# Kernel tuning notes

Hardware: AMD Instinct MI355X
Metric: run time of the kernel (lower is better)

The kernel has to match this reference:

```python
import jax, jax.numpy as jnp
import numpy as np

N = 10000   # num nodes
E = 160000  # num edges (avg degree 16)
B = 8       # batch dim carried on node state
D = 64      # hidden_size


def setup_inputs() -> dict:
    key = jax.random.key(0)
    k1, k2, k3, k4, k5, k6 = jax.random.split(key, 6)
    state = jax.random.normal(k1, (N, B, D), jnp.float32)
    feature = jax.random.normal(k2, (N, 32), jnp.float32)  # unused by GAT math, kept for call signature
    weight = jax.random.normal(k3, (2 * D, D), jnp.float32) * 0.05
    src = jax.random.randint(k4, (E,), 0, N, jnp.int32)
    dst = jax.random.randint(k5, (E,), 0, N, jnp.int32)
    dist = jax.random.uniform(k6, (E, 1), jnp.float32)
    return dict(state=state, feature=feature, weight=weight, src=src, dst=dst, dist=dist)


def reference(state, feature, weight, src, dst, dist):
    # --- msg_edge: gather src/dst node states per edge ---
    src_state = state[src]                 # [E,B,D]
    dst_state = state[dst]                 # [E,B,D]
    es = jnp.concatenate([src_state, dst_state], axis=-1)          # [E,B,2D]
    alpha = jax.nn.leaky_relu(jnp.einsum('ebk,kd->ebd', es, weight),
                              negative_slope=0.2)                  # tf.nn.leaky_relu alpha=0.2
    alpha = alpha * dist[:, :, None]       # dist [E,1] broadcast to [E,1,1]

    # --- msg_reduce: segment softmax over incoming edges of each dst node ---
    amax = jax.ops.segment_max(alpha, dst, num_segments=N)         # [N,B,D]
    ex = jnp.exp(alpha - amax[dst])                                # stable exp
    denom = jax.ops.segment_sum(ex, dst, num_segments=N)           # [N,B,D]
    attn = ex / denom[dst]                                         # [E,B,D]

    # weighted sum of src states scattered back to dst nodes, then relu
    new_state = jax.nn.relu(jax.ops.segment_sum(attn * src_state, dst, num_segments=N))
    return new_state
```

## Files before the change

### kernel.cpp

```cpp
#include <hip/hip_runtime.h>
#include <hip/hip_fp16.h>
#include <math.h>

#define N_NODES 10000
#define N_EDGES 160000
#define B_ 8
#define D_ 64
#define BD 512
#define ROWS 80000
#define SLICE 640000
#define CAP 48

typedef _Float16 f16x8 __attribute__((ext_vector_type(8)));
typedef float f32x4 __attribute__((ext_vector_type(4)));
typedef float f4v __attribute__((ext_vector_type(4)));
typedef unsigned int u32;

union HU { _Float16 f; unsigned short u; };
union HC { u32 u; __half2 h; };

__global__ void __launch_bounds__(256) prep_kernel(
    const int* __restrict__ src, const int* __restrict__ dst,
    const float* __restrict__ dist, int* __restrict__ counts, u32* __restrict__ bucket,
    const float* __restrict__ state, const float* __restrict__ weight,
    __half2* __restrict__ G, __half* __restrict__ Pd) {
    __shared__ _Float16 At[64 * 72];
    __shared__ _Float16 Bt[128 * 72];
    int bid = blockIdx.x;
    int tid = threadIdx.x;

    if (bid < 625) {
        int e = bid * 256 + tid;
        int s = __builtin_nontemporal_load(&src[e]);
        int d = __builtin_nontemporal_load(&dst[e]);
        float di = __builtin_nontemporal_load(&dist[e]);
        int pos = atomicAdd(&counts[d], 1);
        if (pos < CAP) {
            unsigned short hd = __half_as_ushort(__float2half_rn(di * 1.44269504f));
            bucket[d * CAP + pos] = (u32)s | ((u32)hd << 16);
        }
        return;
    }

    int row0 = (bid - 625) * 64;

    const f4v* st4 = (const f4v*)(state + (size_t)row0 * 64);
    for (int i = tid; i < 1024; i += 256) {
        int r = i >> 4, c4 = (i & 15) << 2;
        f4v v = __builtin_nontemporal_load(&st4[i]);
        union { short4 s; _Float16 h[4]; } u;
        u.h[0] = (_Float16)v[0]; u.h[1] = (_Float16)v[1];
        u.h[2] = (_Float16)v[2]; u.h[3] = (_Float16)v[3];
        *(short4*)&At[r * 72 + c4] = u.s;
    }
    const f4v* w4 = (const f4v*)weight;
    for (int i = tid; i < 2048; i += 256) {
        int r = i >> 4, c4 = (i & 15) << 2;
        f4v v = w4[i];
        int h = r >> 6, k = r & 63;
        int nb = h * 64 + c4;
        Bt[(nb + 0) * 72 + k] = (_Float16)v[0];
        Bt[(nb + 1) * 72 + k] = (_Float16)v[1];
        Bt[(nb + 2) * 72 + k] = (_Float16)v[2];
        Bt[(nb + 3) * 72 + k] = (_Float16)v[3];
    }
    __syncthreads();

    int wave = tid >> 6, lane = tid & 63;
    int quad = lane >> 4, m16 = lane & 15;
    int m_loc = wave * 16 + m16;

    f16x8 a0 = *(const f16x8*)&At[m_loc * 72 + quad * 8];
    f16x8 a1 = *(const f16x8*)&At[m_loc * 72 + 32 + quad * 8];

#pragma unroll
    for (int tcol = 0; tcol < 8; tcol++) {
        int n = tcol * 16 + m16;
        f16x8 b0 = *(const f16x8*)&Bt[n * 72 + quad * 8];
        f16x8 b1 = *(const f16x8*)&Bt[n * 72 + 32 + quad * 8];
        f32x4 acc = {0.f, 0.f, 0.f, 0.f};
        acc = __builtin_amdgcn_mfma_f32_16x16x32_f16(a0, b0, acc, 0, 0, 0);
        acc = __builtin_amdgcn_mfma_f32_16x16x32_f16(a1, b1, acc, 0, 0, 0);
#pragma unroll
        for (int r = 0; r < 4; r++) {
            int ml = wave * 16 + quad * 4 + r;
            int m = row0 + ml;
            int node = m >> 3, bb = m & 7;
            size_t base = (size_t)bb * SLICE + (size_t)node * 64;
            if (tcol < 4) {
                HU xu; xu.f = At[ml * 72 + n];
                ushort2 pk;
                pk.x = __half_as_ushort(__float2half_rn(acc[r]));
                pk.y = xu.u;
                *(ushort2*)&G[base + n] = pk;
            } else {
                Pd[base + (n - 64)] = __float2half_rn(acc[r]);
            }
        }
    }
}

__global__ void __launch_bounds__(256) gat_aggregate(
    const __half2* __restrict__ G,
    const __half* __restrict__ Pds,
    const int* __restrict__ counts,
    const u32* __restrict__ bucket,
    float* __restrict__ out) {
    int bid = blockIdx.x;
    int b = bid & 7;
    int grp = bid >> 3;
    int wave = threadIdx.x >> 6;
    int lane = threadIdx.x & 63;
    int n = (grp << 2) + wave;
    int eidx = lane >> 4;
    int lpart = lane & 15;

    const __half2* Gb = G + (size_t)b * SLICE;
    const __half* Pb = Pds + (size_t)b * SLICE;

    union { double d; __half2 h[2]; } pdu;
    pdu.d = __builtin_nontemporal_load((const double*)(Pb + n * 64 + lpart * 4));
    __half2 pd01 = pdu.h[0], pd23 = pdu.h[1];

    int cnt = counts[n];
    if (cnt > CAP) cnt = CAP;
    const u32* ep = bucket + n * CAP;

    const __half2 c06 = __float2half2_rn(0.6f);
    const __half2 c04 = __float2half2_rn(0.4f);
    const u32 ABSM = 0x7fff7fffu;

    __half2 l01 = __float2half2_rn(0.f), l23 = l01;
    __half2 o01 = l01, o23 = l01;

    if (cnt > 0) {
        int last = cnt - 1;
        int idx = eidx <= last ? eidx : last;
        u32 rec = __builtin_nontemporal_load(&ep[idx]);
        float4 g = *(const float4*)(Gb + (size_t)(rec & 0xffffu) * 64 + lpart * 4);
        __half hdd = __ushort_as_half((unsigned short)(rec >> 16));
        __half2 ddl = __halves2half2(hdd, hdd);
        int j = 0;
        for (;;) {
            int jn = j + 4;
            bool more = jn < cnt;
            float4 g2; __half2 ddl2;
            if (more) {
                int i2 = jn + eidx; i2 = i2 <= last ? i2 : last;
                u32 rec2 = __builtin_nontemporal_load(&ep[i2]);
                g2 = *(const float4*)(Gb + (size_t)(rec2 & 0xffffu) * 64 + lpart * 4);
                __half h2 = __ushort_as_half((unsigned short)(rec2 >> 16));
                ddl2 = __halves2half2(h2, h2);
            }
            bool act = (j + eidx) <= last;
            union { float4 f; __half2 h[4]; } gu; gu.f = g;
            __half2 p01 = __halves2half2(__low2half(gu.h[0]), __low2half(gu.h[1]));
            __half2 p23 = __halves2half2(__low2half(gu.h[2]), __low2half(gu.h[3]));
            __half2 x01 = __halves2half2(__high2half(gu.h[0]), __high2half(gu.h[1]));
            __half2 x23 = __halves2half2(__high2half(gu.h[2]), __high2half(gu.h[3]));
            __half2 z01 = __hadd2(p01, pd01);
            __half2 z23 = __hadd2(p23, pd23);
            HC az01, az23, zz01, zz23;
            zz01.h = z01; zz23.h = z23;
            az01.u = zz01.u & ABSM;
            az23.u = zz23.u & ABSM;
            __half2 lk01 = __hfma2(az01.h, c04, __hmul2(z01, c06));
            __half2 lk23 = __hfma2(az23.h, c04, __hmul2(z23, c06));
            __half2 a01 = __hmul2(lk01, ddl);
            __half2 a23 = __hmul2(lk23, ddl);
            __half2 e01 = __halves2half2(hexp2(__low2half(a01)), hexp2(__high2half(a01)));
            __half2 e23 = __halves2half2(hexp2(__low2half(a23)), hexp2(__high2half(a23)));
            HC s01, s23;
            s01.h = e01; s23.h = e23;
            s01.u = act ? s01.u : 0u;
            s23.u = act ? s23.u : 0u;
            l01 = __hadd2(l01, s01.h);
            l23 = __hadd2(l23, s23.h);
            o01 = __hfma2(s01.h, x01, o01);
            o23 = __hfma2(s23.h, x23, o23);
            if (!more) break;
            j = jn; g = g2; ddl = ddl2;
        }
#pragma unroll
        for (int m = 16; m <= 32; m <<= 1) {
            HC c;
            c.u = (u32)__shfl_xor((int)((HC){.h = l01}).u, m, 64); l01 = __hadd2(l01, c.h);
            c.u = (u32)__shfl_xor((int)((HC){.h = l23}).u, m, 64); l23 = __hadd2(l23, c.h);
            c.u = (u32)__shfl_xor((int)((HC){.h = o01}).u, m, 64); o01 = __hadd2(o01, c.h);
            c.u = (u32)__shfl_xor((int)((HC){.h = o23}).u, m, 64); o23 = __hadd2(o23, c.h);
        }
    }
    if (eidx == 0) {
        f4v r;
        if (cnt > 0) {
            float l0 = __low2float(l01), l1 = __high2float(l01);
            float l2 = __low2float(l23), l3 = __high2float(l23);
            float o0 = __low2float(o01), o1 = __high2float(o01);
            float o2 = __low2float(o23), o3 = __high2float(o23);
            r[0] = fmaxf(o0 * __builtin_amdgcn_rcpf(l0), 0.f);
            r[1] = fmaxf(o1 * __builtin_amdgcn_rcpf(l1), 0.f);
            r[2] = fmaxf(o2 * __builtin_amdgcn_rcpf(l2), 0.f);
            r[3] = fmaxf(o3 * __builtin_amdgcn_rcpf(l3), 0.f);
        } else {
            r[0] = 0.f; r[1] = 0.f; r[2] = 0.f; r[3] = 0.f;
        }
        f4v* dst4 = (f4v*)(out + (size_t)n * BD + b * 64 + lpart * 4);
        __builtin_nontemporal_store(r, dst4);
    }
}

extern "C" void kernel_launch(void* const* d_in, const int* in_sizes, int n_in,
                              void* d_out, int out_size, void* d_ws, size_t ws_size,
                              hipStream_t stream) {
    const float* state  = (const float*)d_in[0];
    const float* weight = (const float*)d_in[2];
    const int*   src    = (const int*)d_in[3];
    const int*   dst    = (const int*)d_in[4];
    const float* dist   = (const float*)d_in[5];

    __half2* G      = (__half2*)d_ws;
    __half*  Pd     = (__half*)(G + (size_t)8 * SLICE);
    u32*     bucket = (u32*)(Pd + (size_t)8 * SLICE);
    int*     counts = (int*)(bucket + (size_t)N_NODES * CAP);

    hipMemsetAsync(counts, 0, N_NODES * sizeof(int), stream);
    prep_kernel<<<1875, 256, 0, stream>>>(src, dst, dist, counts, bucket,
                                          state, weight, G, Pd);
    gat_aggregate<<<N_NODES * 2, 256, 0, stream>>>(G, Pd, counts, bucket, (float*)d_out);
}
```

Baseline: 164.3 us.

## Stage GEMM outputs in LDS for vector stores, unroll gather by eight edges

The prep kernel now writes MFMA results into shared-memory tiles and then emits coalesced 16-byte stores to G and Pd, replacing scattered 4-byte and 2-byte stores. The aggregate kernel handles eight edges per iteration with two in-flight gathers per lane, raising memory-level parallelism at the cost of more registers. Nontemporal load and store hints are dropped in favour of ordinary loads and stores. The extra shared memory (24 KB) may lower occupancy of the prep kernel.

```diff
diff --git a/kernel.cpp b/kernel.cpp
--- a/kernel.cpp
+++ b/kernel.cpp
@@ -26,14 +26,16 @@
     __half2* __restrict__ G, __half* __restrict__ Pd) {
     __shared__ _Float16 At[64 * 72];
     __shared__ _Float16 Bt[128 * 72];
+    __shared__ u32 Gs[64 * 64];
+    __shared__ unsigned short Ps[64 * 64];
     int bid = blockIdx.x;
     int tid = threadIdx.x;
 
     if (bid < 625) {
         int e = bid * 256 + tid;
-        int s = __builtin_nontemporal_load(&src[e]);
-        int d = __builtin_nontemporal_load(&dst[e]);
-        float di = __builtin_nontemporal_load(&dist[e]);
+        int s = src[e];
+        int d = dst[e];
+        float di = dist[e];
         int pos = atomicAdd(&counts[d], 1);
         if (pos < CAP) {
             unsigned short hd = __half_as_ushort(__float2half_rn(di * 1.44269504f));
@@ -84,19 +86,28 @@
 #pragma unroll
         for (int r = 0; r < 4; r++) {
             int ml = wave * 16 + quad * 4 + r;
-            int m = row0 + ml;
-            int node = m >> 3, bb = m & 7;
-            size_t base = (size_t)bb * SLICE + (size_t)node * 64;
             if (tcol < 4) {
                 HU xu; xu.f = At[ml * 72 + n];
-                ushort2 pk;
-                pk.x = __half_as_ushort(__float2half_rn(acc[r]));
-                pk.y = xu.u;
-                *(ushort2*)&G[base + n] = pk;
+                Gs[ml * 64 + n] = (u32)__half_as_ushort(__float2half_rn(acc[r]))
+                                  | ((u32)xu.u << 16);
             } else {
-                Pd[base + (n - 64)] = __float2half_rn(acc[r]);
+                Ps[ml * 64 + (n - 64)] = __half_as_ushort(__float2half_rn(acc[r]));
             }
         }
+    }
+    __syncthreads();
+
+    for (int i = tid; i < 1024; i += 256) {
+        int row = i >> 4, seg = i & 15;
+        int m = row0 + row;
+        size_t base = (size_t)(m & 7) * SLICE + (size_t)(m >> 3) * 64;
+        *(float4*)&G[base + seg * 4] = *(const float4*)&Gs[row * 64 + seg * 4];
+    }
+    for (int i = tid; i < 512; i += 256) {
+        int row = i >> 3, seg = i & 7;
+        int m = row0 + row;
+        size_t base = (size_t)(m & 7) * SLICE + (size_t)(m >> 3) * 64;
+        *(float4*)&Pd[base + seg * 8] = *(const float4*)&Ps[row * 64 + seg * 8];
     }
 }
 
@@ -119,7 +130,7 @@
     const __half* Pb = Pds + (size_t)b * SLICE;
 
     union { double d; __half2 h[2]; } pdu;
-    pdu.d = __builtin_nontemporal_load((const double*)(Pb + n * 64 + lpart * 4));
+    pdu.d = *(const double*)(Pb + n * 64 + lpart * 4);
     __half2 pd01 = pdu.h[0], pd23 = pdu.h[1];
 
     int cnt = counts[n];
@@ -135,51 +146,67 @@
 
     if (cnt > 0) {
         int last = cnt - 1;
-        int idx = eidx <= last ? eidx : last;
-        u32 rec = __builtin_nontemporal_load(&ep[idx]);
-        float4 g = *(const float4*)(Gb + (size_t)(rec & 0xffffu) * 64 + lpart * 4);
-        __half hdd = __ushort_as_half((unsigned short)(rec >> 16));
-        __half2 ddl = __halves2half2(hdd, hdd);
+        int iA = eidx <= last ? eidx : last;
+        int iB = (4 + eidx) <= last ? (4 + eidx) : last;
+        u32 recA = ep[iA];
+        u32 recB = ep[iB];
+        float4 gA = *(const float4*)(Gb + (size_t)(recA & 0xffffu) * 64 + lpart * 4);
+        float4 gB = *(const float4*)(Gb + (size_t)(recB & 0xffffu) * 64 + lpart * 4);
+        __half hA = __ushort_as_half((unsigned short)(recA >> 16));
+        __half hB = __ushort_as_half((unsigned short)(recB >> 16));
+        __half2 dA = __halves2half2(hA, hA);
+        __half2 dB = __halves2half2(hB, hB);
+
         int j = 0;
         for (;;) {
-            int jn = j + 4;
+            int jn = j + 8;
             bool more = jn < cnt;
-            float4 g2; __half2 ddl2;
+            float4 gA2, gB2; __half2 dA2, dB2;
             if (more) {
-                int i2 = jn + eidx; i2 = i2 <= last ? i2 : last;
-                u32 rec2 = __builtin_nontemporal_load(&ep[i2]);
-                g2 = *(const float4*)(Gb + (size_t)(rec2 & 0xffffu) * 64 + lpart * 4);
-                __half h2 = __ushort_as_half((unsigned short)(rec2 >> 16));
-                ddl2 = __halves2half2(h2, h2);
+                int a2 = jn + eidx;      a2 = a2 <= last ? a2 : last;
+                int b2 = jn + 4 + eidx;  b2 = b2 <= last ? b2 : last;
+                u32 rA2 = ep[a2];
+                u32 rB2 = ep[b2];
+                gA2 = *(const float4*)(Gb + (size_t)(rA2 & 0xffffu) * 64 + lpart * 4);
+                gB2 = *(const float4*)(Gb + (size_t)(rB2 & 0xffffu) * 64 + lpart * 4);
+                __half h2a = __ushort_as_half((unsigned short)(rA2 >> 16));
+                __half h2b = __ushort_as_half((unsigned short)(rB2 >> 16));
+                dA2 = __halves2half2(h2a, h2a);
+                dB2 = __halves2half2(h2b, h2b);
             }
-            bool act = (j + eidx) <= last;
-            union { float4 f; __half2 h[4]; } gu; gu.f = g;
-            __half2 p01 = __halves2half2(__low2half(gu.h[0]), __low2half(gu.h[1]));
-            __half2 p23 = __halves2half2(__low2half(gu.h[2]), __low2half(gu.h[3]));
-            __half2 x01 = __halves2half2(__high2half(gu.h[0]), __high2half(gu.h[1]));
-            __half2 x23 = __halves2half2(__high2half(gu.h[2]), __high2half(gu.h[3]));
-            __half2 z01 = __hadd2(p01, pd01);
-            __half2 z23 = __hadd2(p23, pd23);
-            HC az01, az23, zz01, zz23;
-            zz01.h = z01; zz23.h = z23;
-            az01.u = zz01.u & ABSM;
-            az23.u = zz23.u & ABSM;
-            __half2 lk01 = __hfma2(az01.h, c04, __hmul2(z01, c06));
-            __half2 lk23 = __hfma2(az23.h, c04, __hmul2(z23, c06));
-            __half2 a01 = __hmul2(lk01, ddl);
-            __half2 a23 = __hmul2(lk23, ddl);
-            __half2 e01 = __halves2half2(hexp2(__low2half(a01)), hexp2(__high2half(a01)));
-            __half2 e23 = __halves2half2(hexp2(__low2half(a23)), hexp2(__high2half(a23)));
-            HC s01, s23;
-            s01.h = e01; s23.h = e23;
-            s01.u = act ? s01.u : 0u;
-            s23.u = act ? s23.u : 0u;
-            l01 = __hadd2(l01, s01.h);
-            l23 = __hadd2(l23, s23.h);
-            o01 = __hfma2(s01.h, x01, o01);
-            o23 = __hfma2(s23.h, x23, o23);
+#pragma unroll
+            for (int c = 0; c < 2; c++) {
+                bool act = (j + c * 4 + eidx) <= last;
+                float4 g = c == 0 ? gA : gB;
+                __half2 ddl = c == 0 ? dA : dB;
+                union { float4 f; __half2 h[4]; } gu; gu.f = g;
+                __half2 p01 = __halves2half2(__low2half(gu.h[0]), __low2half(gu.h[1]));
+                __half2 p23 = __halves2half2(__low2half(gu.h[2]), __low2half(gu.h[3]));
+                __half2 x01 = __halves2half2(__high2half(gu.h[0]), __high2half(gu.h[1]));
+                __half2 x23 = __halves2half2(__high2half(gu.h[2]), __high2half(gu.h[3]));
+                __half2 z01 = __hadd2(p01, pd01);
+                __half2 z23 = __hadd2(p23, pd23);
+                HC az01, az23, zz01, zz23;
+                zz01.h = z01; zz23.h = z23;
+                az01.u = zz01.u & ABSM;
+                az23.u = zz23.u & ABSM;
+                __half2 lk01 = __hfma2(az01.h, c04, __hmul2(z01, c06));
+                __half2 lk23 = __hfma2(az23.h, c04, __hmul2(z23, c06));
+                __half2 a01 = __hmul2(lk01, ddl);
+                __half2 a23 = __hmul2(lk23, ddl);
+                __half2 e01 = __halves2half2(hexp2(__low2half(a01)), hexp2(__high2half(a01)));
+                __half2 e23 = __halves2half2(hexp2(__low2half(a23)), hexp2(__high2half(a23)));
+                HC s01, s23;
+                s01.h = e01; s23.h = e23;
+                s01.u = act ? s01.u : 0u;
+                s23.u = act ? s23.u : 0u;
+                l01 = __hadd2(l01, s01.h);
+                l23 = __hadd2(l23, s23.h);
+                o01 = __hfma2(s01.h, x01, o01);
+                o23 = __hfma2(s23.h, x23, o23);
+            }
             if (!more) break;
-            j = jn; g = g2; ddl = ddl2;
+            j = jn; gA = gA2; gB = gB2; dA = dA2; dB = dB2;
         }
 #pragma unroll
         for (int m = 16; m <= 32; m <<= 1) {
@@ -191,21 +218,20 @@
         }
     }
     if (eidx == 0) {
-        f4v r;
+        float4 r;
         if (cnt > 0) {
             float l0 = __low2float(l01), l1 = __high2float(l01);
             float l2 = __low2float(l23), l3 = __high2float(l23);
             float o0 = __low2float(o01), o1 = __high2float(o01);
             float o2 = __low2float(o23), o3 = __high2float(o23);
-            r[0] = fmaxf(o0 * __builtin_amdgcn_rcpf(l0), 0.f);
-            r[1] = fmaxf(o1 * __builtin_amdgcn_rcpf(l1), 0.f);
-            r[2] = fmaxf(o2 * __builtin_amdgcn_rcpf(l2), 0.f);
-            r[3] = fmaxf(o3 * __builtin_amdgcn_rcpf(l3), 0.f);
+            r.x = fmaxf(o0 * __builtin_amdgcn_rcpf(l0), 0.f);
+            r.y = fmaxf(o1 * __builtin_amdgcn_rcpf(l1), 0.f);
+            r.z = fmaxf(o2 * __builtin_amdgcn_rcpf(l2), 0.f);
+            r.w = fmaxf(o3 * __builtin_amdgcn_rcpf(l3), 0.f);
         } else {
-            r[0] = 0.f; r[1] = 0.f; r[2] = 0.f; r[3] = 0.f;
-        }
-        f4v* dst4 = (f4v*)(out + (size_t)n * BD + b * 64 + lpart * 4);
-        __builtin_nontemporal_store(r, dst4);
+            r = make_float4(0.f, 0.f, 0.f, 0.f);
+        }
+        *(float4*)(out + (size_t)n * BD + b * 64 + lpart * 4) = r;
     }
 }
 
```

After: 155.1 us. 5.6% less time.
